# Optimization experiments

Hardware: AMD Instinct MI355X
Metric: run time of the kernel (lower is better)

## Reference

```python
import jax, jax.numpy as jnp
import numpy as np

N, E = 20000, 100000          # nodes, edges
H = 64                        # node_hidden_dim (== node_input_dim)
EIN, EH = 16, 128             # edge_input_dim, edge_hidden_dim
STEPS = 3                     # num_steps


def setup_inputs() -> dict:
    key = jax.random.key(0)
    ks = jax.random.split(key, 10)
    s = 0.05
    return {
        "node_features": jax.random.normal(ks[0], (N, H), jnp.float32),
        "edge_attr": jax.random.normal(ks[1], (E, EIN), jnp.float32),
        "edge_index": jax.random.randint(ks[2], (2, E), 0, N),
        # mp_input: Linear(H, H)
        "mp_w": jax.random.normal(ks[3], (H, H), jnp.float32) * s,
        "mp_b": jnp.zeros((H,), jnp.float32),
        # message_layer: Linear(2H, H)
        "msg_w": jax.random.normal(ks[4], (H, 2 * H), jnp.float32) * s,
        "msg_b": jnp.zeros((H,), jnp.float32),
        # edge network: Linear(EIN, EH) -> ReLU -> Linear(EH, H*H)
        "e1_w": jax.random.normal(ks[5], (EH, EIN), jnp.float32) * s,
        "e1_b": jnp.zeros((EH,), jnp.float32),
        "e2_w": jax.random.normal(ks[6], (H * H, EH), jnp.float32) * s,
        "e2_b": jnp.zeros((H * H,), jnp.float32),
        # NNConv root weight and bias
        "root": jax.random.normal(ks[7], (H, H), jnp.float32) * s,
        "conv_b": jnp.zeros((H,), jnp.float32),
    }


def reference(node_features, edge_attr, edge_index,
              mp_w, mp_b, msg_w, msg_b,
              e1_w, e1_b, e2_w, e2_b, root, conv_b):
    src, dst = edge_index[0], edge_index[1]
    out = jax.nn.relu(node_features @ mp_w.T + mp_b)  # [N, H]
    # Edge-conditioned weight matrices; edge_attr is constant across steps so
    # the edge MLP output is identical each step -> compute once (same math).
    W_e = (jax.nn.relu(edge_attr @ e1_w.T + e1_b) @ e2_w.T + e2_b).reshape(E, H, H)
    for _ in range(STEPS):
        # gather src features, per-edge matmul, scatter-add to dst
        msgs = jnp.einsum('ei,eio->eo', out[src], W_e)          # [E, H]
        agg = jax.ops.segment_sum(msgs, dst, num_segments=N)    # [N, H]
        m = jax.nn.relu(agg + out @ root + conv_b)              # NNConv + ReLU
        out = jnp.concatenate([m, out], axis=1) @ msg_w.T + msg_b
    return out + node_features
```

## Files before the change

### kernel.cpp

```cpp
#include <hip/hip_runtime.h>

#define N_ 20000
#define E_ 100000

typedef __attribute__((ext_vector_type(8))) short short8;
typedef __attribute__((ext_vector_type(4))) float f32x4;

__device__ __forceinline__ unsigned short f2bf(float f) {
  union { float f; unsigned u; } v; v.f = f;
  unsigned r = v.u + 0x7fffu + ((v.u >> 16) & 1u);
  return (unsigned short)(r >> 16);
}
__device__ __forceinline__ float bf2f(unsigned short h) {
  union { unsigned u; float f; } v; v.u = ((unsigned)h) << 16;
  return v.f;
}
__device__ __forceinline__ short8 pack8(float4 a, float4 b) {
  short8 v;
  v[0] = (short)f2bf(a.x); v[1] = (short)f2bf(a.y);
  v[2] = (short)f2bf(a.z); v[3] = (short)f2bf(a.w);
  v[4] = (short)f2bf(b.x); v[5] = (short)f2bf(b.y);
  v[6] = (short)f2bf(b.z); v[7] = (short)f2bf(b.w);
  return v;
}

__global__ __launch_bounds__(256) void k_h2(const float* __restrict__ ea,
                                            const float* __restrict__ e1w,
                                            const float* __restrict__ e1b,
                                            unsigned short* __restrict__ h2) {
  int t = threadIdx.x, w = t >> 6, l = t & 63, g = l >> 4, lm = l & 15;
  short8 bf[8];
#pragma unroll
  for (int cf = 0; cf < 8; ++cf) {
    int c = cf * 16 + lm;
    short8 v = {0, 0, 0, 0, 0, 0, 0, 0};
    if (g < 2) {
      const float4* wp = (const float4*)(e1w + c * 16 + g * 8);
      v = pack8(wp[0], wp[1]);
    } else if (g == 2) {
      v[0] = (short)f2bf(e1b[c]);
    }
    bf[cf] = v;
  }
  const f32x4 z = {0.f, 0.f, 0.f, 0.f};
  for (int tile = 0; tile < 4; ++tile) {
    int e0 = blockIdx.x * 256 + tile * 64 + w * 16;
    if (e0 >= E_) break;
    int er = e0 + lm; if (er >= E_) er = E_ - 1;
    short8 a = {0, 0, 0, 0, 0, 0, 0, 0};
    if (g < 2) {
      const float4* ap = (const float4*)(ea + er * 16 + g * 8);
      a = pack8(ap[0], ap[1]);
    } else if (g == 2) {
      a[0] = (short)0x3F80;
    }
#pragma unroll
    for (int cf = 0; cf < 8; ++cf) {
      f32x4 acc = __builtin_amdgcn_mfma_f32_16x16x32_bf16(a, bf[cf], z, 0, 0, 0);
#pragma unroll
      for (int r = 0; r < 4; ++r) {
        int e = e0 + g * 4 + r;
        if (e < E_) h2[(size_t)e * 128 + cf * 16 + lm] = f2bf(fmaxf(acc[r], 0.f));
      }
    }
  }
}

__global__ __launch_bounds__(256) void k_prep_bf(const float* __restrict__ e2w,
                                                 unsigned short* __restrict__ Af) {
  int tid = blockIdx.x * 256 + threadIdx.x;
  int l = tid & 63, kf = (tid >> 6) & 3, ct = tid >> 8;
  int gq = l >> 4, lm = l & 15;
  const float* src = e2w + (ct * 16 + lm) * 128 + kf * 32 + gq * 8;
  short8 v = pack8(*(const float4*)src, *(const float4*)(src + 4));
  *(short8*)((short*)Af + (size_t)tid * 8) = v;
}

__global__ __launch_bounds__(256) void k_node_in(const float* __restrict__ nfm,
                                                 const float* __restrict__ mpw,
                                                 const float* __restrict__ mpb,
                                                 const float* __restrict__ e2b,
                                                 float* __restrict__ outc,
                                                 float* __restrict__ yc) {
  __shared__ float wT[64 * 65];
  __shared__ float xr[4 * 65];
  __shared__ float nr[4 * 65];
  int t = threadIdx.x;
  for (int idx = t; idx < 4096; idx += 256) {
    int o = idx >> 6, i = idx & 63;
    wT[i * 65 + o] = mpw[idx];
  }
  __syncthreads();
  int nl = t >> 6, o = t & 63;
  for (int it = 0; it < 16; ++it) {
    int n = blockIdx.x * 64 + it * 4 + nl;
    bool ok = n < N_;
    int nc = ok ? n : N_ - 1;
    xr[nl * 65 + o] = nfm[(size_t)nc * 64 + o];
    __syncthreads();
    float acc = mpb[o];
#pragma unroll 8
    for (int i = 0; i < 64; ++i) acc += xr[nl * 65 + i] * wT[i * 65 + o];
    float m = fmaxf(acc, 0.f);
    if (ok) outc[(size_t)n * 64 + o] = m;
    nr[nl * 65 + o] = m;
    __syncthreads();
    float yv = 0.f;
#pragma unroll 8
    for (int j = 0; j < 64; ++j) yv += nr[nl * 65 + j] * e2b[j * 64 + o];
    if (ok) yc[(size_t)n * 64 + o] = yv;
    __syncthreads();
  }
}

__global__ void k_zero(float* __restrict__ p, int n) {
  int i = blockIdx.x * 256 + threadIdx.x;
  if (i < n) p[i] = 0.f;
}

__global__ __launch_bounds__(256, 3) void k_msgs(const float* __restrict__ x,
                                                 const float* __restrict__ y,
                                                 const unsigned short* __restrict__ h2,
                                                 const unsigned short* __restrict__ Af,
                                                 const int* __restrict__ ei,
                                                 float* __restrict__ agg) {
  __shared__ __align__(16) unsigned char POOL[33792];
  __shared__ int sidx[128];
  __shared__ int didx[128];
  int t = threadIdx.x, w = t >> 6, l = t & 63;
  int op = w >> 1, kh = w & 1;
  int gq = l >> 4, lm = l & 15;
  int e0 = blockIdx.x * 128;
  if (t < 128) {
    int e = e0 + t;
    sidx[t] = (e < E_) ? ei[e] : 0;
    didx[t] = (e < E_) ? ei[E_ + e] : -1;
  }
  __syncthreads();
  int kb = 2 * kh;
  short8 hf[8][2];
#pragma unroll
  for (int ef = 0; ef < 8; ++ef) {
    int e = e0 + ef * 16 + lm;
    if (e >= E_) e = E_ - 1;
    const short8* hp = (const short8*)(h2 + (size_t)e * 128 + gq * 8);
    hf[ef][0] = hp[(kb + 0) * 4];
    hf[ef][1] = hp[(kb + 1) * 4];
  }
  float* xg = (float*)POOL;
  {
    int e = t >> 1, h = t & 1;
    const float* xr = x + (size_t)sidx[e] * 64 + h * 32;
#pragma unroll
    for (int q = 0; q < 8; ++q) {
      float4 v = *(const float4*)(xr + q * 4);
      int ib = h * 32 + q * 4;
      xg[(ib + 0) * 132 + e] = v.x;
      xg[(ib + 1) * 132 + e] = v.y;
      xg[(ib + 2) * 132 + e] = v.z;
      xg[(ib + 3) * 132 + e] = v.w;
    }
  }
  __syncthreads();

  f32x4 macc[8][2];
#pragma unroll
  for (int ef = 0; ef < 8; ++ef) {
    macc[ef][0] = f32x4{0.f, 0.f, 0.f, 0.f};
    macc[ef][1] = f32x4{0.f, 0.f, 0.f, 0.f};
  }
  const f32x4 z = {0.f, 0.f, 0.f, 0.f};
  const short8* As = (const short8*)Af;
  int fb = 2 * op;

  for (int i = 0; i < 64; ++i) {
    int ct0 = i * 4 + fb;
    const short8* p0 = As + (size_t)(ct0 * 4 + kb) * 64 + l;
    short8 w00 = p0[0];
    short8 w01 = p0[64];
    short8 w10 = p0[256];
    short8 w11 = p0[320];
#pragma unroll
    for (int ef = 0; ef < 8; ++ef) {
      float xs = xg[i * 132 + ef * 16 + lm];
      f32x4 d0, d1;
      d0 = __builtin_amdgcn_mfma_f32_16x16x32_bf16(w00, hf[ef][0], z, 0, 0, 0);
      d1 = __builtin_amdgcn_mfma_f32_16x16x32_bf16(w10, hf[ef][0], z, 0, 0, 0);
      d0 = __builtin_amdgcn_mfma_f32_16x16x32_bf16(w01, hf[ef][1], d0, 0, 0, 0);
      d1 = __builtin_amdgcn_mfma_f32_16x16x32_bf16(w11, hf[ef][1], d1, 0, 0, 0);
      macc[ef][0] += xs * d0;
      macc[ef][1] += xs * d1;
    }
  }
  __syncthreads();
  unsigned short* pm = (unsigned short*)POOL;
#pragma unroll
  for (int ef = 0; ef < 8; ++ef)
#pragma unroll
    for (int oql = 0; oql < 2; ++oql)
#pragma unroll
      for (int r = 0; r < 4; ++r)
        pm[kh * 8448 + (ef * 16 + lm) * 66 + op * 32 + oql * 16 + gq * 4 + r] =
            f2bf(macc[ef][oql][r]);
  __syncthreads();
  for (int it = 0; it < 32; ++it) {
    int idx = it * 256 + t;
    int e = idx >> 6, o = idx & 63;
    int d = didx[e];
    if (d >= 0) {
      float v = bf2f(pm[e * 66 + o]) + bf2f(pm[8448 + e * 66 + o]);
      v += y[(size_t)sidx[e] * 64 + o];
      atomicAdd(agg + (size_t)d * 64 + o, v);
    }
  }
}

__global__ __launch_bounds__(256) void k_update(const float* __restrict__ outc,
                                                float* __restrict__ agg,
                                                const float* __restrict__ root,
                                                const float* __restrict__ convb,
                                                const float* __restrict__ msgw,
                                                const float* __restrict__ msgb,
                                                const float* __restrict__ e2b,
                                                const float* __restrict__ nfm,
                                                int last,
                                                float* __restrict__ outn,
                                                float* __restrict__ yn,
                                                float* __restrict__ dout) {
  __shared__ float wT[128 * 65];
  __shared__ float xr[4 * 65];
  __shared__ float mr[4 * 65];
  __shared__ float nr[4 * 65];
  int t = threadIdx.x;
  for (int idx = t; idx < 8192; idx += 256) {
    int o = idx >> 7, j = idx & 127;
    wT[j * 65 + o] = msgw[idx];
  }
  __syncthreads();
  int nl = t >> 6, o = t & 63;
  for (int it = 0; it < 16; ++it) {
    int n = blockIdx.x * 64 + it * 4 + nl;
    bool ok = n < N_;
    int nc = ok ? n : N_ - 1;
    xr[nl * 65 + o] = outc[(size_t)nc * 64 + o];
    __syncthreads();
    float acc = agg[(size_t)nc * 64 + o] + convb[o];
    if (ok) agg[(size_t)n * 64 + o] = 0.f;
#pragma unroll 8
    for (int i = 0; i < 64; ++i) acc += xr[nl * 65 + i] * root[i * 64 + o];
    float m = fmaxf(acc, 0.f);
    mr[nl * 65 + o] = m;
    __syncthreads();
    float o2 = msgb[o];
#pragma unroll 8
    for (int j = 0; j < 64; ++j)
      o2 += mr[nl * 65 + j] * wT[j * 65 + o] + xr[nl * 65 + j] * wT[(64 + j) * 65 + o];
    nr[nl * 65 + o] = o2;
    __syncthreads();
    if (last) {
      if (ok) dout[(size_t)n * 64 + o] = o2 + nfm[(size_t)n * 64 + o];
    } else {
      float yv = 0.f;
#pragma unroll 8
      for (int j = 0; j < 64; ++j) yv += nr[nl * 65 + j] * e2b[j * 64 + o];
      if (ok) {
        outn[(size_t)n * 64 + o] = o2;
        yn[(size_t)n * 64 + o] = yv;
      }
    }
    __syncthreads();
  }
}

extern "C" void kernel_launch(void* const* d_in, const int* in_sizes, int n_in,
                              void* d_out, int out_size, void* d_ws, size_t ws_size,
                              hipStream_t stream) {
  const float* nfm  = (const float*)d_in[0];
  const float* ea   = (const float*)d_in[1];
  const int*   ei   = (const int*)d_in[2];
  const float* mpw  = (const float*)d_in[3];
  const float* mpb  = (const float*)d_in[4];
  const float* msgw = (const float*)d_in[5];
  const float* msgb = (const float*)d_in[6];
  const float* e1w  = (const float*)d_in[7];
  const float* e1b  = (const float*)d_in[8];
  const float* e2w  = (const float*)d_in[9];
  const float* e2b  = (const float*)d_in[10];
  const float* root = (const float*)d_in[11];
  const float* convb= (const float*)d_in[12];
  float* out = (float*)d_out;

  char* ws = (char*)d_ws;
  unsigned short* h2 = (unsigned short*)ws; ws += (size_t)E_ * 128 * 2;
  unsigned short* Af = (unsigned short*)ws; ws += (size_t)4096 * 128 * 2;
  float* outa = (float*)ws; ws += (size_t)N_ * 64 * 4;
  float* ya   = (float*)ws; ws += (size_t)N_ * 64 * 4;
  float* outb = (float*)ws; ws += (size_t)N_ * 64 * 4;
  float* yb   = (float*)ws; ws += (size_t)N_ * 64 * 4;
  float* agg  = (float*)ws; ws += (size_t)N_ * 64 * 4;

  hipLaunchKernelGGL(k_prep_bf, dim3(256), dim3(256), 0, stream, e2w, Af);
  hipLaunchKernelGGL(k_zero, dim3((N_ * 64 + 255) / 256), dim3(256), 0, stream, agg, N_ * 64);
  hipLaunchKernelGGL(k_h2, dim3((E_ + 255) / 256), dim3(256), 0, stream, ea, e1w, e1b, h2);
  hipLaunchKernelGGL(k_node_in, dim3((N_ + 63) / 64), dim3(256), 0, stream, nfm, mpw, mpb, e2b, outa, ya);

  float* oc = outa; float* yc = ya; float* on = outb; float* yv = yb;
  for (int s = 0; s < 3; ++s) {
    hipLaunchKernelGGL(k_msgs, dim3((E_ + 127) / 128), dim3(256), 0, stream, oc, yc, h2, Af, ei, agg);
    hipLaunchKernelGGL(k_update, dim3((N_ + 63) / 64), dim3(256), 0, stream, oc, agg, root, convb,
                       msgw, msgb, e2b, nfm, (s == 2) ? 1 : 0, on, yv, out);
    float* tp;
    tp = oc; oc = on; on = tp;
    tp = yc; yc = yv; yv = tp;
  }
}
```

Baseline: 763.3 us.

## Merge prep kernels, prefetch weights in k_msgs, drop per-row barriers in update

Folds the four setup kernels (weight packing, node input transform, edge hidden layer, agg zeroing) into one launch that branches on block ranges, removing three launch gaps. In the message kernel, the next iteration's weight fragments and gathered x values are loaded one step ahead (register double buffering) so their latency overlaps the MFMA work. The node update and node-input kernels now give each wavefront its own rows and use wave-private LDS scratch, so the per-row __syncthreads go away; root and e2b are staged in LDS and read as float4. Register pressure in k_msgs rises and may hurt occupancy at the 3-blocks-per-SM bound.

```diff
diff --git a/kernel.cpp b/kernel.cpp
--- a/kernel.cpp
+++ b/kernel.cpp
@@ -24,98 +24,120 @@
   return v;
 }
 
-__global__ __launch_bounds__(256) void k_h2(const float* __restrict__ ea,
-                                            const float* __restrict__ e1w,
-                                            const float* __restrict__ e1b,
-                                            unsigned short* __restrict__ h2) {
-  int t = threadIdx.x, w = t >> 6, l = t & 63, g = l >> 4, lm = l & 15;
-  short8 bf[8];
-#pragma unroll
-  for (int cf = 0; cf < 8; ++cf) {
-    int c = cf * 16 + lm;
-    short8 v = {0, 0, 0, 0, 0, 0, 0, 0};
-    if (g < 2) {
-      const float4* wp = (const float4*)(e1w + c * 16 + g * 8);
-      v = pack8(wp[0], wp[1]);
-    } else if (g == 2) {
-      v[0] = (short)f2bf(e1b[c]);
-    }
-    bf[cf] = v;
-  }
-  const f32x4 z = {0.f, 0.f, 0.f, 0.f};
-  for (int tile = 0; tile < 4; ++tile) {
-    int e0 = blockIdx.x * 256 + tile * 64 + w * 16;
-    if (e0 >= E_) break;
-    int er = e0 + lm; if (er >= E_) er = E_ - 1;
-    short8 a = {0, 0, 0, 0, 0, 0, 0, 0};
-    if (g < 2) {
-      const float4* ap = (const float4*)(ea + er * 16 + g * 8);
-      a = pack8(ap[0], ap[1]);
-    } else if (g == 2) {
-      a[0] = (short)0x3F80;
-    }
+#define PREP_B 256
+#define NODEIN_B 313
+#define H2_B 391
+#define ZERO_B 128
+
+__global__ __launch_bounds__(256) void k_pre(const float* __restrict__ e2w,
+                                             unsigned short* __restrict__ Af,
+                                             const float* __restrict__ nfm,
+                                             const float* __restrict__ mpw,
+                                             const float* __restrict__ mpb,
+                                             const float* __restrict__ e2b,
+                                             float* __restrict__ outc,
+                                             float* __restrict__ yc,
+                                             const float* __restrict__ ea,
+                                             const float* __restrict__ e1w,
+                                             const float* __restrict__ e1b,
+                                             unsigned short* __restrict__ h2,
+                                             float* __restrict__ agg) {
+  __shared__ float SH[9088];
+  int bid = blockIdx.x, t = threadIdx.x;
+  if (bid < PREP_B) {
+    int tid = bid * 256 + t;
+    int l = tid & 63, kf = (tid >> 6) & 3, ct = tid >> 8;
+    int gq = l >> 4, lm = l & 15;
+    const float* src = e2w + (ct * 16 + lm) * 128 + kf * 32 + gq * 8;
+    short8 v = pack8(*(const float4*)src, *(const float4*)(src + 4));
+    *(short8*)((short*)Af + (size_t)tid * 8) = v;
+    return;
+  }
+  bid -= PREP_B;
+  if (bid < NODEIN_B) {
+    float* wS = SH;
+    float* eS = SH + 4160;
+    float* rows = SH + 8320;
+    for (int idx = t; idx < 4096; idx += 256) {
+      int o = idx >> 6, i = idx & 63;
+      wS[i * 65 + o] = mpw[idx];
+      eS[i * 65 + o] = e2b[i * 64 + o];
+    }
+    __syncthreads();
+    int w = t >> 6, o = t & 63;
+    float* rx = rows + w * 192;
+    float bo = mpb[o];
+    for (int q = 0; q < 16; ++q) {
+      int n = bid * 64 + w * 16 + q;
+      if (n >= N_) break;
+      rx[o] = nfm[(size_t)n * 64 + o];
+      float acc = bo;
+#pragma unroll
+      for (int i4 = 0; i4 < 16; ++i4) {
+        float4 xq = *(float4*)(rx + i4 * 4);
+        acc += xq.x * wS[(i4 * 4 + 0) * 65 + o] + xq.y * wS[(i4 * 4 + 1) * 65 + o] +
+               xq.z * wS[(i4 * 4 + 2) * 65 + o] + xq.w * wS[(i4 * 4 + 3) * 65 + o];
+      }
+      float m = fmaxf(acc, 0.f);
+      outc[(size_t)n * 64 + o] = m;
+      rx[64 + o] = m;
+      float yv = 0.f;
+#pragma unroll
+      for (int j4 = 0; j4 < 16; ++j4) {
+        float4 mq = *(float4*)(rx + 64 + j4 * 4);
+        yv += mq.x * eS[(j4 * 4 + 0) * 65 + o] + mq.y * eS[(j4 * 4 + 1) * 65 + o] +
+              mq.z * eS[(j4 * 4 + 2) * 65 + o] + mq.w * eS[(j4 * 4 + 3) * 65 + o];
+      }
+      yc[(size_t)n * 64 + o] = yv;
+    }
+    return;
+  }
+  bid -= NODEIN_B;
+  if (bid < H2_B) {
+    int w = t >> 6, l = t & 63, g = l >> 4, lm = l & 15;
+    short8 bf[8];
 #pragma unroll
     for (int cf = 0; cf < 8; ++cf) {
-      f32x4 acc = __builtin_amdgcn_mfma_f32_16x16x32_bf16(a, bf[cf], z, 0, 0, 0);
-#pragma unroll
-      for (int r = 0; r < 4; ++r) {
-        int e = e0 + g * 4 + r;
-        if (e < E_) h2[(size_t)e * 128 + cf * 16 + lm] = f2bf(fmaxf(acc[r], 0.f));
-      }
-    }
-  }
-}
-
-__global__ __launch_bounds__(256) void k_prep_bf(const float* __restrict__ e2w,
-                                                 unsigned short* __restrict__ Af) {
-  int tid = blockIdx.x * 256 + threadIdx.x;
-  int l = tid & 63, kf = (tid >> 6) & 3, ct = tid >> 8;
-  int gq = l >> 4, lm = l & 15;
-  const float* src = e2w + (ct * 16 + lm) * 128 + kf * 32 + gq * 8;
-  short8 v = pack8(*(const float4*)src, *(const float4*)(src + 4));
-  *(short8*)((short*)Af + (size_t)tid * 8) = v;
-}
-
-__global__ __launch_bounds__(256) void k_node_in(const float* __restrict__ nfm,
-                                                 const float* __restrict__ mpw,
-                                                 const float* __restrict__ mpb,
-                                                 const float* __restrict__ e2b,
-                                                 float* __restrict__ outc,
-                                                 float* __restrict__ yc) {
-  __shared__ float wT[64 * 65];
-  __shared__ float xr[4 * 65];
-  __shared__ float nr[4 * 65];
-  int t = threadIdx.x;
-  for (int idx = t; idx < 4096; idx += 256) {
-    int o = idx >> 6, i = idx & 63;
-    wT[i * 65 + o] = mpw[idx];
-  }
-  __syncthreads();
-  int nl = t >> 6, o = t & 63;
-  for (int it = 0; it < 16; ++it) {
-    int n = blockIdx.x * 64 + it * 4 + nl;
-    bool ok = n < N_;
-    int nc = ok ? n : N_ - 1;
-    xr[nl * 65 + o] = nfm[(size_t)nc * 64 + o];
-    __syncthreads();
-    float acc = mpb[o];
-#pragma unroll 8
-    for (int i = 0; i < 64; ++i) acc += xr[nl * 65 + i] * wT[i * 65 + o];
-    float m = fmaxf(acc, 0.f);
-    if (ok) outc[(size_t)n * 64 + o] = m;
-    nr[nl * 65 + o] = m;
-    __syncthreads();
-    float yv = 0.f;
-#pragma unroll 8
-    for (int j = 0; j < 64; ++j) yv += nr[nl * 65 + j] * e2b[j * 64 + o];
-    if (ok) yc[(size_t)n * 64 + o] = yv;
-    __syncthreads();
-  }
-}
-
-__global__ void k_zero(float* __restrict__ p, int n) {
-  int i = blockIdx.x * 256 + threadIdx.x;
-  if (i < n) p[i] = 0.f;
+      int c = cf * 16 + lm;
+      short8 v = {0, 0, 0, 0, 0, 0, 0, 0};
+      if (g < 2) {
+        const float4* wp = (const float4*)(e1w + c * 16 + g * 8);
+        v = pack8(wp[0], wp[1]);
+      } else if (g == 2) {
+        v[0] = (short)f2bf(e1b[c]);
+      }
+      bf[cf] = v;
+    }
+    const f32x4 z = {0.f, 0.f, 0.f, 0.f};
+    for (int tile = 0; tile < 4; ++tile) {
+      int e0 = bid * 256 + tile * 64 + w * 16;
+      if (e0 >= E_) break;
+      int er = e0 + lm; if (er >= E_) er = E_ - 1;
+      short8 a = {0, 0, 0, 0, 0, 0, 0, 0};
+      if (g < 2) {
+        const float4* ap = (const float4*)(ea + er * 16 + g * 8);
+        a = pack8(ap[0], ap[1]);
+      } else if (g == 2) {
+        a[0] = (short)0x3F80;
+      }
+#pragma unroll
+      for (int cf = 0; cf < 8; ++cf) {
+        f32x4 acc = __builtin_amdgcn_mfma_f32_16x16x32_bf16(a, bf[cf], z, 0, 0, 0);
+#pragma unroll
+        for (int r = 0; r < 4; ++r) {
+          int e = e0 + g * 4 + r;
+          if (e < E_) h2[(size_t)e * 128 + cf * 16 + lm] = f2bf(fmaxf(acc[r], 0.f));
+        }
+      }
+    }
+    return;
+  }
+  bid -= H2_B;
+  {
+    float4* p = (float4*)agg;
+    const float4 z4 = {0.f, 0.f, 0.f, 0.f};
+    for (int idx = bid * 256 + t; idx < N_ * 16; idx += ZERO_B * 256) p[idx] = z4;
+  }
 }
 
 __global__ __launch_bounds__(256, 3) void k_msgs(const float* __restrict__ x,
@@ -173,24 +195,32 @@
   const short8* As = (const short8*)Af;
   int fb = 2 * op;
 
+  const short8* p0 = As + (size_t)((0 * 4 + fb) * 4 + kb) * 64 + l;
+  short8 c00 = p0[0], c01 = p0[64], c10 = p0[256], c11 = p0[320];
+  float xc[8];
+#pragma unroll
+  for (int ef = 0; ef < 8; ++ef) xc[ef] = xg[0 * 132 + ef * 16 + lm];
+
   for (int i = 0; i < 64; ++i) {
-    int ct0 = i * 4 + fb;
-    const short8* p0 = As + (size_t)(ct0 * 4 + kb) * 64 + l;
-    short8 w00 = p0[0];
-    short8 w01 = p0[64];
-    short8 w10 = p0[256];
-    short8 w11 = p0[320];
+    int ip = (i + 1) & 63;
+    const short8* pn = As + (size_t)((ip * 4 + fb) * 4 + kb) * 64 + l;
+    short8 n00 = pn[0], n01 = pn[64], n10 = pn[256], n11 = pn[320];
+    float xn[8];
+#pragma unroll
+    for (int ef = 0; ef < 8; ++ef) xn[ef] = xg[ip * 132 + ef * 16 + lm];
 #pragma unroll
     for (int ef = 0; ef < 8; ++ef) {
-      float xs = xg[i * 132 + ef * 16 + lm];
       f32x4 d0, d1;
-      d0 = __builtin_amdgcn_mfma_f32_16x16x32_bf16(w00, hf[ef][0], z, 0, 0, 0);
-      d1 = __builtin_amdgcn_mfma_f32_16x16x32_bf16(w10, hf[ef][0], z, 0, 0, 0);
-      d0 = __builtin_amdgcn_mfma_f32_16x16x32_bf16(w01, hf[ef][1], d0, 0, 0, 0);
-      d1 = __builtin_amdgcn_mfma_f32_16x16x32_bf16(w11, hf[ef][1], d1, 0, 0, 0);
-      macc[ef][0] += xs * d0;
-      macc[ef][1] += xs * d1;
-    }
+      d0 = __builtin_amdgcn_mfma_f32_16x16x32_bf16(c00, hf[ef][0], z, 0, 0, 0);
+      d1 = __builtin_amdgcn_mfma_f32_16x16x32_bf16(c10, hf[ef][0], z, 0, 0, 0);
+      d0 = __builtin_amdgcn_mfma_f32_16x16x32_bf16(c01, hf[ef][1], d0, 0, 0, 0);
+      d1 = __builtin_amdgcn_mfma_f32_16x16x32_bf16(c11, hf[ef][1], d1, 0, 0, 0);
+      macc[ef][0] += xc[ef] * d0;
+      macc[ef][1] += xc[ef] * d1;
+    }
+    c00 = n00; c01 = n01; c10 = n10; c11 = n11;
+#pragma unroll
+    for (int ef = 0; ef < 8; ++ef) xc[ef] = xn[ef];
   }
   __syncthreads();
   unsigned short* pm = (unsigned short*)POOL;
@@ -227,48 +257,63 @@
                                                 float* __restrict__ outn,
                                                 float* __restrict__ yn,
                                                 float* __restrict__ dout) {
-  __shared__ float wT[128 * 65];
-  __shared__ float xr[4 * 65];
-  __shared__ float mr[4 * 65];
-  __shared__ float nr[4 * 65];
+  __shared__ float SH[17408];
+  float* wS = SH;
+  float* rS = SH + 8320;
+  float* eS = SH + 12480;
+  float* rows = SH + 16640;
   int t = threadIdx.x;
   for (int idx = t; idx < 8192; idx += 256) {
     int o = idx >> 7, j = idx & 127;
-    wT[j * 65 + o] = msgw[idx];
-  }
-  __syncthreads();
-  int nl = t >> 6, o = t & 63;
-  for (int it = 0; it < 16; ++it) {
-    int n = blockIdx.x * 64 + it * 4 + nl;
-    bool ok = n < N_;
-    int nc = ok ? n : N_ - 1;
-    xr[nl * 65 + o] = outc[(size_t)nc * 64 + o];
-    __syncthreads();
-    float acc = agg[(size_t)nc * 64 + o] + convb[o];
-    if (ok) agg[(size_t)n * 64 + o] = 0.f;
-#pragma unroll 8
-    for (int i = 0; i < 64; ++i) acc += xr[nl * 65 + i] * root[i * 64 + o];
+    wS[j * 65 + o] = msgw[idx];
+  }
+  for (int idx = t; idx < 4096; idx += 256) {
+    int i = idx >> 6, o = idx & 63;
+    rS[i * 65 + o] = root[idx];
+    eS[i * 65 + o] = e2b[idx];
+  }
+  __syncthreads();
+  int w = t >> 6, o = t & 63;
+  float* rx = rows + w * 192;
+  float cb = convb[o], mb = msgb[o];
+  for (int q = 0; q < 16; ++q) {
+    int n = blockIdx.x * 64 + w * 16 + q;
+    if (n >= N_) break;
+    rx[o] = outc[(size_t)n * 64 + o];
+    float acc = agg[(size_t)n * 64 + o] + cb;
+    agg[(size_t)n * 64 + o] = 0.f;
+#pragma unroll
+    for (int i4 = 0; i4 < 16; ++i4) {
+      float4 xq = *(float4*)(rx + i4 * 4);
+      acc += xq.x * rS[(i4 * 4 + 0) * 65 + o] + xq.y * rS[(i4 * 4 + 1) * 65 + o] +
+             xq.z * rS[(i4 * 4 + 2) * 65 + o] + xq.w * rS[(i4 * 4 + 3) * 65 + o];
+    }
     float m = fmaxf(acc, 0.f);
-    mr[nl * 65 + o] = m;
-    __syncthreads();
-    float o2 = msgb[o];
-#pragma unroll 8
-    for (int j = 0; j < 64; ++j)
-      o2 += mr[nl * 65 + j] * wT[j * 65 + o] + xr[nl * 65 + j] * wT[(64 + j) * 65 + o];
-    nr[nl * 65 + o] = o2;
-    __syncthreads();
+    rx[64 + o] = m;
+    float o2 = mb;
+#pragma unroll
+    for (int j4 = 0; j4 < 16; ++j4) {
+      float4 mq = *(float4*)(rx + 64 + j4 * 4);
+      float4 xq = *(float4*)(rx + j4 * 4);
+      o2 += mq.x * wS[(j4 * 4 + 0) * 65 + o] + mq.y * wS[(j4 * 4 + 1) * 65 + o] +
+            mq.z * wS[(j4 * 4 + 2) * 65 + o] + mq.w * wS[(j4 * 4 + 3) * 65 + o];
+      o2 += xq.x * wS[(64 + j4 * 4 + 0) * 65 + o] + xq.y * wS[(64 + j4 * 4 + 1) * 65 + o] +
+            xq.z * wS[(64 + j4 * 4 + 2) * 65 + o] + xq.w * wS[(64 + j4 * 4 + 3) * 65 + o];
+    }
     if (last) {
-      if (ok) dout[(size_t)n * 64 + o] = o2 + nfm[(size_t)n * 64 + o];
+      dout[(size_t)n * 64 + o] = o2 + nfm[(size_t)n * 64 + o];
     } else {
+      rx[128 + o] = o2;
       float yv = 0.f;
-#pragma unroll 8
-      for (int j = 0; j < 64; ++j) yv += nr[nl * 65 + j] * e2b[j * 64 + o];
-      if (ok) {
-        outn[(size_t)n * 64 + o] = o2;
-        yn[(size_t)n * 64 + o] = yv;
-      }
-    }
-    __syncthreads();
+#pragma unroll
+      for (int j4 = 0; j4 < 16; ++j4) {
+        float4 nq = *(float4*)(rx + 128 + j4 * 4);
+        yv += nq.x * eS[(j4 * 4 + 0) * 65 + o] + nq.y * eS[(j4 * 4 + 1) * 65 + o] +
+              nq.z * eS[(j4 * 4 + 2) * 65 + o] + nq.w * eS[(j4 * 4 + 3) * 65 + o];
+      }
+      outn[(size_t)n * 64 + o] = o2;
+      yn[(size_t)n * 64 + o] = yv;
+    }
   }
 }
 
@@ -299,10 +344,8 @@
   float* yb   = (float*)ws; ws += (size_t)N_ * 64 * 4;
   float* agg  = (float*)ws; ws += (size_t)N_ * 64 * 4;
 
-  hipLaunchKernelGGL(k_prep_bf, dim3(256), dim3(256), 0, stream, e2w, Af);
-  hipLaunchKernelGGL(k_zero, dim3((N_ * 64 + 255) / 256), dim3(256), 0, stream, agg, N_ * 64);
-  hipLaunchKernelGGL(k_h2, dim3((E_ + 255) / 256), dim3(256), 0, stream, ea, e1w, e1b, h2);
-  hipLaunchKernelGGL(k_node_in, dim3((N_ + 63) / 64), dim3(256), 0, stream, nfm, mpw, mpb, e2b, outa, ya);
+  hipLaunchKernelGGL(k_pre, dim3(PREP_B + NODEIN_B + H2_B + ZERO_B), dim3(256), 0, stream,
+                     e2w, Af, nfm, mpw, mpb, e2b, outa, ya, ea, e1w, e1b, h2, agg);
 
   float* oc = outa; float* yc = ya; float* on = outb; float* yv = yb;
   for (int s = 0; s < 3; ++s) {
```

New measurement: 762.1 us. About the same (-0.2%).
